# Optimization experiments

Measured on AMD Instinct MI355X. Metric: run time of the kernel, lower is better.

Reference implementation:

```python
import jax, jax.numpy as jnp
import numpy as np

B, C, H, W = 2048, 4, 84, 84
FEAT = 7 * 7 * 64  # 3136, from 84->20->9->7 conv arithmetic
D = 512
E = 6            # num_experts
K = 2            # top_k
A = 12           # output_dim (actions)


def _conv(x, w, b, stride):
    y = jax.lax.conv_general_dilated(
        x, w, window_strides=(stride, stride), padding='VALID',
        dimension_numbers=('NCHW', 'OIHW', 'NCHW'))
    return y + b[None, :, None, None]


def setup_inputs() -> dict:
    key = jax.random.key(0)
    ks = jax.random.split(key, 16)
    s = lambda k, shape, fan: jax.random.normal(k, shape, jnp.float32) * (1.0 / np.sqrt(fan))
    return {
        'x': jax.random.normal(ks[0], (B, C, H, W), jnp.float32),
        'c1_w': s(ks[1], (32, C, 8, 8), C * 64), 'c1_b': jnp.zeros((32,), jnp.float32),
        'c2_w': s(ks[2], (64, 32, 4, 4), 32 * 16), 'c2_b': jnp.zeros((64,), jnp.float32),
        'c3_w': s(ks[3], (64, 64, 3, 3), 64 * 9), 'c3_b': jnp.zeros((64,), jnp.float32),
        'fc_w': s(ks[4], (FEAT, D), FEAT), 'fc_b': jnp.zeros((D,), jnp.float32),
        'gate_w': s(ks[5], (D, E), D), 'gate_b': jnp.zeros((E,), jnp.float32),
        'e_w1': s(ks[6], (E, D, D), D), 'e_b1': jnp.zeros((E, D), jnp.float32),
        'e_w2': s(ks[7], (E, D, D), D), 'e_b2': jnp.zeros((E, D), jnp.float32),
        'e_w3': s(ks[8], (E, D, A), D), 'e_b3': jnp.zeros((E, A), jnp.float32),
    }


def reference(x, c1_w, c1_b, c2_w, c2_b, c3_w, c3_b, fc_w, fc_b,
              gate_w, gate_b, e_w1, e_b1, e_w2, e_b2, e_w3, e_b3):
    # CNN feature extractor (dropout omitted: eval semantics)
    h = jax.nn.relu(_conv(x, c1_w, c1_b, 4))
    h = jax.nn.relu(_conv(h, c2_w, c2_b, 2))
    h = jax.nn.relu(_conv(h, c3_w, c3_b, 1))
    h = h.reshape(h.shape[0], -1)                     # [B, 3136] (C,H,W flatten order)
    f = jax.nn.relu(h @ fc_w + fc_b)                  # [B, 512]

    # Gating: softmax -> top-2 -> renormalize
    gate_probs = jax.nn.softmax(f @ gate_w + gate_b, axis=-1)    # [B, E]
    top_p, top_i = jax.lax.top_k(gate_probs, K)                   # [B, K]
    top_p = top_p / jnp.sum(top_p, axis=-1, keepdims=True)

    # Experts: compute all (tiny MLPs), then gather top-k outputs
    h1 = jax.nn.relu(jnp.einsum('bd,edh->beh', f, e_w1) + e_b1)   # [B, E, D]
    h2 = jax.nn.relu(jnp.einsum('beh,ehg->beg', h1, e_w2) + e_b2) # [B, E, D]
    eo = jnp.einsum('beg,ego->beo', h2, e_w3) + e_b3              # [B, E, A]
    sel = jnp.take_along_axis(eo, top_i[:, :, None], axis=1)      # [B, K, A]
    out = jnp.sum(sel * top_p[:, :, None], axis=1)                # [B, A]
    return out
```

## Files before the change

### kernel.cpp

```cpp
#include <hip/hip_runtime.h>
#include <hip/hip_bf16.h>
#include <math.h>

typedef __attribute__((ext_vector_type(8))) short bf16x8;
typedef __attribute__((ext_vector_type(4))) float f32x4;

__device__ __forceinline__ float b2f(unsigned short u) {
    unsigned int v = ((unsigned int)u) << 16;
    return __uint_as_float(v);
}
__device__ __forceinline__ unsigned short f2b(float f) {
    __hip_bfloat16 h = __float2bfloat16(f);
    return *reinterpret_cast<unsigned short*>(&h);
}
__device__ __forceinline__ void split_trunc(float v, short& h, short& l) {
    unsigned int ui = __float_as_uint(v);
    h = (short)(ui >> 16);
    float hf = __uint_as_float(ui & 0xffff0000u);
    l = (short)f2b(v - hf);
}

__global__ __launch_bounds__(256) void prep_w(
    const float* __restrict__ w1, const float* __restrict__ w2, const float* __restrict__ w3,
    const float* __restrict__ ew3,
    unsigned short* __restrict__ wb1h, unsigned short* __restrict__ wb1l,
    unsigned short* __restrict__ w2h, unsigned short* __restrict__ w2l,
    unsigned short* __restrict__ w3h, unsigned short* __restrict__ w3l,
    float* __restrict__ w3t) {
    int tid = blockIdx.x * 256 + threadIdx.x;
    if (tid < 8192) {
        int k = tid >> 8, r = tid & 255;
        int c = r >> 6, ky = (r >> 3) & 7, kx = r & 7;
        float v = w1[tid];
        unsigned short h = f2b(v);
        int d = ((ky * 2 + (k >> 4)) * 16 + (k & 15)) * 32 + c * 8 + kx;
        wb1h[d] = h;
        wb1l[d] = f2b(v - b2f(h));
    } else if (tid < 8192 + 32768) {
        int i = tid - 8192;
        int n = i >> 9, r = i & 511;
        int c = r >> 4, ky = (r >> 2) & 3, kx = r & 3;
        float v = w2[i];
        unsigned short h = f2b(v);
        int d = ((ky * 4 + kx) * 64 + n) * 32 + c;
        w2h[d] = h;
        w2l[d] = f2b(v - b2f(h));
    } else if (tid < 8192 + 32768 + 36864) {
        int i = tid - 40960;
        int n = i / 576, r = i - n * 576;
        int c = r / 9, s = r - c * 9;
        int ky = s / 3, kx = s - ky * 3;
        float v = w3[i];
        unsigned short h = f2b(v);
        int d = (((ky * 3 + kx) * 2 + (c >> 5)) * 64 + n) * 32 + (c & 31);
        w3h[d] = h;
        w3l[d] = f2b(v - b2f(h));
    } else if (tid < 77824 + 36864) {
        int i = tid - 77824;
        int e = i / 6144, rem = i - e * 6144;
        int a = rem >> 9, k = rem & 511;
        w3t[i] = ew3[e * 6144 + k * 12 + a];
    }
}

__global__ __launch_bounds__(256) void prep_fcw(
    const float* __restrict__ fw, unsigned short* __restrict__ h, unsigned short* __restrict__ l) {
    __shared__ float tile[64][65];
    int k0 = blockIdx.x * 64;
    int n0 = blockIdx.y * 64;
    int tx = threadIdx.x & 63, ty = threadIdx.x >> 6;
#pragma unroll
    for (int j = 0; j < 16; j++) {
        int kk = ty + j * 4;
        int kp = k0 + kk;
        int p = kp >> 6, c = kp & 63;
        tile[kk][tx] = fw[(c * 49 + p) * 512 + n0 + tx];
    }
    __syncthreads();
#pragma unroll
    for (int j = 0; j < 16; j++) {
        int r = ty + j * 4;
        float v = tile[tx][r];
        unsigned short hh = f2b(v);
        long d = (long)(n0 + r) * 3136 + k0 + tx;
        h[d] = hh;
        l[d] = f2b(v - b2f(hh));
    }
}

__global__ __launch_bounds__(256) void prep_ewT(
    const float* __restrict__ ew1, const float* __restrict__ ew2,
    unsigned short* __restrict__ t1, unsigned short* __restrict__ t2) {
    __shared__ float tile[32][33];
    int z = blockIdx.z;
    int e = z % 6;
    const float* src = (z < 6) ? (ew1 + e * 262144) : (ew2 + e * 262144);
    unsigned short* dst = (z < 6) ? (t1 + e * 262144) : (t2 + e * 262144);
    int d0 = blockIdx.y * 32;
    int h0 = blockIdx.x * 32;
    int tx = threadIdx.x, ty = threadIdx.y;
#pragma unroll
    for (int j = 0; j < 4; j++)
        tile[ty + j * 8][tx] = src[(d0 + ty + j * 8) * 512 + h0 + tx];
    __syncthreads();
#pragma unroll
    for (int j = 0; j < 4; j++)
        dst[(h0 + ty + j * 8) * 512 + (d0 + tx)] = f2b(tile[tx][ty + j * 8]);
}

__global__ __launch_bounds__(256, 3) void conv1_k(
    const float* __restrict__ x, const unsigned short* __restrict__ wbh,
    const unsigned short* __restrict__ wbl, const float* __restrict__ b1,
    unsigned short* __restrict__ yhi, unsigned short* __restrict__ ylo) {
    int t = threadIdx.x;
    int wave = t >> 6, lane = t & 63, l16 = lane & 15, quad = lane >> 4;
    int px0 = blockIdx.x * 256 + wave * 64;
    const float* abase[4];
#pragma unroll
    for (int i = 0; i < 4; i++) {
        int px = px0 + i * 16 + l16;
        int n = px / 400;
        int rem = px - n * 400;
        int oy = rem / 20;
        int ox = rem - oy * 20;
        abase[i] = x + (long)n * 28224 + quad * 7056 + oy * 4 * 84 + ox * 4;
    }
    f32x4 acc[4][2];
#pragma unroll
    for (int i = 0; i < 4; i++)
#pragma unroll
        for (int j = 0; j < 2; j++)
#pragma unroll
            for (int r = 0; r < 4; r++) acc[i][j][r] = 0.f;
    float4 cur[8];
#pragma unroll
    for (int i = 0; i < 4; i++) {
        cur[i * 2] = *(const float4*)abase[i];
        cur[i * 2 + 1] = *(const float4*)(abase[i] + 4);
    }
#pragma unroll
    for (int ky = 0; ky < 8; ky++) {
        float4 nxt[8];
        if (ky < 7) {
#pragma unroll
            for (int i = 0; i < 4; i++) {
                const float* p = abase[i] + (ky + 1) * 84;
                nxt[i * 2] = *(const float4*)p;
                nxt[i * 2 + 1] = *(const float4*)(p + 4);
            }
        }
        int wo = (ky * 32 + l16) * 32 + quad * 8;
        bf16x8 bh0 = *(const bf16x8*)(wbh + wo);
        bf16x8 bh1 = *(const bf16x8*)(wbh + wo + 512);
        bf16x8 bl0 = *(const bf16x8*)(wbl + wo);
        bf16x8 bl1 = *(const bf16x8*)(wbl + wo + 512);
        bf16x8 ah[4], al[4];
#pragma unroll
        for (int i = 0; i < 4; i++) {
            float v[8] = {cur[i * 2].x, cur[i * 2].y, cur[i * 2].z, cur[i * 2].w,
                          cur[i * 2 + 1].x, cur[i * 2 + 1].y, cur[i * 2 + 1].z, cur[i * 2 + 1].w};
#pragma unroll
            for (int j = 0; j < 8; j++) {
                short hh, ll;
                split_trunc(v[j], hh, ll);
                ah[i][j] = hh;
                al[i][j] = ll;
            }
        }
#pragma unroll
        for (int i = 0; i < 4; i++) {
            acc[i][0] = __builtin_amdgcn_mfma_f32_16x16x32_bf16(ah[i], bh0, acc[i][0], 0, 0, 0);
            acc[i][0] = __builtin_amdgcn_mfma_f32_16x16x32_bf16(al[i], bh0, acc[i][0], 0, 0, 0);
            acc[i][0] = __builtin_amdgcn_mfma_f32_16x16x32_bf16(ah[i], bl0, acc[i][0], 0, 0, 0);
            acc[i][1] = __builtin_amdgcn_mfma_f32_16x16x32_bf16(ah[i], bh1, acc[i][1], 0, 0, 0);
            acc[i][1] = __builtin_amdgcn_mfma_f32_16x16x32_bf16(al[i], bh1, acc[i][1], 0, 0, 0);
            acc[i][1] = __builtin_amdgcn_mfma_f32_16x16x32_bf16(ah[i], bl1, acc[i][1], 0, 0, 0);
        }
        if (ky < 7) {
#pragma unroll
            for (int q = 0; q < 8; q++) cur[q] = nxt[q];
        }
    }
    float bias0 = b1[l16], bias1 = b1[16 + l16];
#pragma unroll
    for (int i = 0; i < 4; i++) {
#pragma unroll
        for (int r = 0; r < 4; r++) {
            long px = px0 + i * 16 + quad * 4 + r;
            long o = px * 32;
            float v0 = fmaxf(acc[i][0][r] + bias0, 0.f);
            float v1 = fmaxf(acc[i][1][r] + bias1, 0.f);
            short h0, l0, h1, l1;
            split_trunc(v0, h0, l0);
            split_trunc(v1, h1, l1);
            yhi[o + l16] = (unsigned short)h0;
            ylo[o + l16] = (unsigned short)l0;
            yhi[o + 16 + l16] = (unsigned short)h1;
            ylo[o + 16 + l16] = (unsigned short)l1;
        }
    }
}

template <int C, int IH, int IW, int OH, int OW, int S, int KH, int KW>
__global__ __launch_bounds__(64, 3) void convm_k(
    const unsigned short* __restrict__ xhi, const unsigned short* __restrict__ xlo,
    const unsigned short* __restrict__ whi, const unsigned short* __restrict__ wlo,
    const float* __restrict__ bias,
    unsigned short* __restrict__ yhi, unsigned short* __restrict__ ylo) {
    constexpr int CH = C / 32;
    constexpr int NCHUNK = KH * KW * CH;
    int lane = threadIdx.x, l16 = lane & 15, quad = lane >> 4;
    int pxbase = blockIdx.x * 64;
    long xoff[4];
#pragma unroll
    for (int i = 0; i < 4; i++) {
        int px = pxbase + i * 16 + l16;
        int n = px / (OH * OW);
        int rem = px - n * (OH * OW);
        int oy = rem / OW;
        int ox = rem - oy * OW;
        xoff[i] = (((long)n * IH + oy * S) * IW + ox * S) * C + quad * 8;
    }
    f32x4 acc[4][4];
#pragma unroll
    for (int i = 0; i < 4; i++)
#pragma unroll
        for (int j = 0; j < 4; j++)
#pragma unroll
            for (int r = 0; r < 4; r++) acc[i][j][r] = 0.f;
#pragma unroll 2
    for (int ck = 0; ck < NCHUNK; ck++) {
        int kyx = ck / CH;
        int ch = ck - kyx * CH;
        int ky = kyx / KW, kx = kyx - ky * KW;
        long koff = ((long)(ky * IW + kx)) * C + ch * 32;
        bf16x8 ah[4], al[4], bh[4], bl[4];
#pragma unroll
        for (int i = 0; i < 4; i++) {
            ah[i] = *(const bf16x8*)(xhi + xoff[i] + koff);
            al[i] = *(const bf16x8*)(xlo + xoff[i] + koff);
        }
#pragma unroll
        for (int j = 0; j < 4; j++) {
            long b = ((long)ck * 64 + j * 16 + l16) * 32 + quad * 8;
            bh[j] = *(const bf16x8*)(whi + b);
            bl[j] = *(const bf16x8*)(wlo + b);
        }
#pragma unroll
        for (int i = 0; i < 4; i++)
#pragma unroll
            for (int j = 0; j < 4; j++) {
                acc[i][j] = __builtin_amdgcn_mfma_f32_16x16x32_bf16(ah[i], bh[j], acc[i][j], 0, 0, 0);
                acc[i][j] = __builtin_amdgcn_mfma_f32_16x16x32_bf16(ah[i], bl[j], acc[i][j], 0, 0, 0);
                acc[i][j] = __builtin_amdgcn_mfma_f32_16x16x32_bf16(al[i], bh[j], acc[i][j], 0, 0, 0);
            }
    }
#pragma unroll
    for (int i = 0; i < 4; i++)
#pragma unroll
        for (int j = 0; j < 4; j++) {
            int col = j * 16 + l16;
            float bv = bias[col];
#pragma unroll
            for (int r = 0; r < 4; r++) {
                int prow = pxbase + i * 16 + quad * 4 + r;
                float v = fmaxf(acc[i][j][r] + bv, 0.f);
                unsigned short h = f2b(v);
                yhi[(long)prow * 64 + col] = h;
                ylo[(long)prow * 64 + col] = f2b(v - b2f(h));
            }
        }
}

__global__ __launch_bounds__(64, 3) void fc_k(
    const unsigned short* __restrict__ Ahi, const unsigned short* __restrict__ Alo,
    const unsigned short* __restrict__ Bhi, const unsigned short* __restrict__ Blo,
    float* __restrict__ Cp) {
    int lane = threadIdx.x, l16 = lane & 15, quad = lane >> 4;
    int m0 = blockIdx.x * 64, n0 = blockIdx.y * 64;
    int z = blockIdx.z;
    int kBase = z * 448;
    f32x4 acc[4][4];
#pragma unroll
    for (int i = 0; i < 4; i++)
#pragma unroll
        for (int j = 0; j < 4; j++)
#pragma unroll
            for (int r = 0; r < 4; r++) acc[i][j][r] = 0.f;
#pragma unroll 2
    for (int k0 = kBase; k0 < kBase + 448; k0 += 32) {
        bf16x8 ah[4], al[4], bh[4], bl[4];
#pragma unroll
        for (int i = 0; i < 4; i++) {
            long a = (long)(m0 + i * 16 + l16) * 3136 + k0 + quad * 8;
            ah[i] = *(const bf16x8*)(Ahi + a);
            al[i] = *(const bf16x8*)(Alo + a);
        }
#pragma unroll
        for (int j = 0; j < 4; j++) {
            long b = (long)(n0 + j * 16 + l16) * 3136 + k0 + quad * 8;
            bh[j] = *(const bf16x8*)(Bhi + b);
            bl[j] = *(const bf16x8*)(Blo + b);
        }
#pragma unroll
        for (int i = 0; i < 4; i++)
#pragma unroll
            for (int j = 0; j < 4; j++) {
                acc[i][j] = __builtin_amdgcn_mfma_f32_16x16x32_bf16(ah[i], bh[j], acc[i][j], 0, 0, 0);
                acc[i][j] = __builtin_amdgcn_mfma_f32_16x16x32_bf16(ah[i], bl[j], acc[i][j], 0, 0, 0);
                acc[i][j] = __builtin_amdgcn_mfma_f32_16x16x32_bf16(al[i], bh[j], acc[i][j], 0, 0, 0);
            }
    }
    float* Cz = Cp + (long)z * 1048576;
#pragma unroll
    for (int i = 0; i < 4; i++)
#pragma unroll
        for (int j = 0; j < 4; j++) {
            int col = n0 + j * 16 + l16;
#pragma unroll
            for (int r = 0; r < 4; r++) {
                int row = m0 + i * 16 + quad * 4 + r;
                Cz[row * 512 + col] = acc[i][j][r];
            }
        }
}

__global__ __launch_bounds__(256) void fc_fin(
    const float* __restrict__ Cp, const float* __restrict__ bias,
    float* __restrict__ f, unsigned short* __restrict__ fb) {
    int tid = blockIdx.x * 256 + threadIdx.x;
    int col = tid & 511;
    float v = bias[col];
#pragma unroll
    for (int z = 0; z < 7; z++) v += Cp[tid + (long)z * 1048576];
    v = fmaxf(v, 0.f);
    f[tid] = v;
    fb[tid] = f2b(v);
}

__global__ __launch_bounds__(256) void gate_k(
    const float* __restrict__ f, const float* __restrict__ gw, const float* __restrict__ gb,
    int* __restrict__ topi, float* __restrict__ topp) {
    int wave = threadIdx.x >> 6, lane = threadIdx.x & 63;
    int row = blockIdx.x * 4 + wave;
    float fv[8];
#pragma unroll
    for (int j = 0; j < 8; j++) fv[j] = f[row * 512 + lane + 64 * j];
    float lg[6];
#pragma unroll
    for (int e = 0; e < 6; e++) {
        float a = 0.f;
#pragma unroll
        for (int j = 0; j < 8; j++) a += fv[j] * gw[(lane + 64 * j) * 6 + e];
#pragma unroll
        for (int off = 32; off > 0; off >>= 1) a += __shfl_xor(a, off, 64);
        lg[e] = a + gb[e];
    }
    if (lane == 0) {
        int i1 = 0;
        float v1 = lg[0];
#pragma unroll
        for (int e = 1; e < 6; e++)
            if (lg[e] > v1) { v1 = lg[e]; i1 = e; }
        int i2 = (i1 == 0) ? 1 : 0;
        float v2 = lg[i2];
#pragma unroll
        for (int e = 0; e < 6; e++)
            if (e != i1 && lg[e] > v2) { v2 = lg[e]; i2 = e; }
        float pa = 1.f / (1.f + expf(v2 - v1));
        topi[row * 2] = i1;
        topi[row * 2 + 1] = i2;
        topp[row * 2] = pa;
        topp[row * 2 + 1] = 1.f - pa;
    }
}

__global__ __launch_bounds__(64, 4) void moe_gemm(
    const unsigned short* __restrict__ A, long aStride,
    const unsigned short* __restrict__ Bt, const float* __restrict__ bias,
    unsigned short* __restrict__ C) {
    int e = blockIdx.z;
    const unsigned short* Ae = A + (long)e * aStride;
    const unsigned short* Be = Bt + (long)e * 262144;
    const float* be = bias + e * 512;
    unsigned short* Ce = C + (long)e * 2048 * 512;
    int lane = threadIdx.x, l16 = lane & 15, quad = lane >> 4;
    int m0 = blockIdx.x * 64, n0 = blockIdx.y * 64;
    f32x4 acc[4][4];
#pragma unroll
    for (int i = 0; i < 4; i++)
#pragma unroll
        for (int j = 0; j < 4; j++)
#pragma unroll
            for (int r = 0; r < 4; r++) acc[i][j][r] = 0.f;
#pragma unroll 4
    for (int k0 = 0; k0 < 512; k0 += 32) {
        bf16x8 a[4], b[4];
#pragma unroll
        for (int i = 0; i < 4; i++)
            a[i] = *(const bf16x8*)(Ae + (long)(m0 + i * 16 + l16) * 512 + k0 + quad * 8);
#pragma unroll
        for (int j = 0; j < 4; j++)
            b[j] = *(const bf16x8*)(Be + (long)(n0 + j * 16 + l16) * 512 + k0 + quad * 8);
#pragma unroll
        for (int i = 0; i < 4; i++)
#pragma unroll
            for (int j = 0; j < 4; j++)
                acc[i][j] = __builtin_amdgcn_mfma_f32_16x16x32_bf16(a[i], b[j], acc[i][j], 0, 0, 0);
    }
#pragma unroll
    for (int i = 0; i < 4; i++)
#pragma unroll
        for (int j = 0; j < 4; j++) {
            int col = n0 + j * 16 + l16;
            float bcol = be[col];
#pragma unroll
            for (int r = 0; r < 4; r++) {
                int row = m0 + i * 16 + quad * 4 + r;
                float v = fmaxf(acc[i][j][r] + bcol, 0.f);
                Ce[(long)row * 512 + col] = f2b(v);
            }
        }
}

__global__ __launch_bounds__(256) void combine_k(
    const unsigned short* __restrict__ h2, const float* __restrict__ w3t,
    const float* __restrict__ b3, const int* __restrict__ topi,
    const float* __restrict__ topp, float* __restrict__ out) {
    int b = blockIdx.x * 4 + (threadIdx.x >> 6);
    int lane = threadIdx.x & 63;
    int e0 = topi[b * 2], e1 = topi[b * 2 + 1];
    float p0 = topp[b * 2], p1 = topp[b * 2 + 1];
    float r[12];
#pragma unroll
    for (int a = 0; a < 12; a++) r[a] = 0.f;
#pragma unroll
    for (int j = 0; j < 2; j++) {
        int e = j ? e1 : e0;
        float p = j ? p1 : p0;
        const unsigned short* hp = h2 + ((long)e * 2048 + b) * 512 + lane * 8;
        bf16x8 hv = *(const bf16x8*)hp;
        float hf[8];
#pragma unroll
        for (int q = 0; q < 8; q++) hf[q] = b2f((unsigned short)hv[q]);
        const float* wb = w3t + e * 6144 + lane * 8;
#pragma unroll
        for (int a = 0; a < 12; a++) {
            float4 w0 = *(const float4*)(wb + a * 512);
            float4 w1 = *(const float4*)(wb + a * 512 + 4);
            float acc = hf[0] * w0.x + hf[1] * w0.y + hf[2] * w0.z + hf[3] * w0.w +
                        hf[4] * w1.x + hf[5] * w1.y + hf[6] * w1.z + hf[7] * w1.w;
            r[a] += p * acc;
        }
    }
#pragma unroll
    for (int a = 0; a < 12; a++)
#pragma unroll
        for (int off = 32; off > 0; off >>= 1) r[a] += __shfl_xor(r[a], off, 64);
    float v = 0.f;
#pragma unroll
    for (int a = 0; a < 12; a++)
        if (lane == a) v = r[a];
    if (lane < 12)
        out[b * 12 + lane] = v + p0 * b3[e0 * 12 + lane] + p1 * b3[e1 * 12 + lane];
}

extern "C" void kernel_launch(void* const* d_in, const int* in_sizes, int n_in,
                              void* d_out, int out_size, void* d_ws, size_t ws_size,
                              hipStream_t stream) {
    const float* x   = (const float*)d_in[0];
    const float* c1w = (const float*)d_in[1];
    const float* c1b = (const float*)d_in[2];
    const float* c2w = (const float*)d_in[3];
    const float* c2b = (const float*)d_in[4];
    const float* c3w = (const float*)d_in[5];
    const float* c3b = (const float*)d_in[6];
    const float* fcw = (const float*)d_in[7];
    const float* fcb = (const float*)d_in[8];
    const float* gw  = (const float*)d_in[9];
    const float* gb  = (const float*)d_in[10];
    const float* ew1 = (const float*)d_in[11];
    const float* eb1 = (const float*)d_in[12];
    const float* ew2 = (const float*)d_in[13];
    const float* eb2 = (const float*)d_in[14];
    const float* ew3 = (const float*)d_in[15];
    const float* eb3 = (const float*)d_in[16];

    char* ws = (char*)d_ws;
    unsigned short* y1hi = (unsigned short*)(ws + 0L);
    unsigned short* y1lo = (unsigned short*)(ws + 52428800L);
    unsigned short* f3hi = (unsigned short*)(ws + 0L);
    unsigned short* f3lo = (unsigned short*)(ws + 12845056L);
    unsigned short* y2hi = (unsigned short*)(ws + 104857600L);
    unsigned short* y2lo = (unsigned short*)(ws + 126091264L);
    unsigned short* h1   = (unsigned short*)(ws + 104857600L);
    unsigned short* h2   = (unsigned short*)(ws + 117440512L);
    float* f             = (float*)(ws + 147324928L);
    unsigned short* fb   = (unsigned short*)(ws + 151519232L);
    int*   topi          = (int*)(ws + 153616384L);
    float* topp          = (float*)(ws + 153632768L);
    unsigned short* w2h  = (unsigned short*)(ws + 153681920L);
    unsigned short* w2l  = (unsigned short*)(ws + 153747456L);
    unsigned short* w3h  = (unsigned short*)(ws + 153812992L);
    unsigned short* w3l  = (unsigned short*)(ws + 153886720L);
    unsigned short* fcwh = (unsigned short*)(ws + 153960448L);
    unsigned short* fcwl = (unsigned short*)(ws + 157171712L);
    unsigned short* ew1t = (unsigned short*)(ws + 160382976L);
    unsigned short* ew2t = (unsigned short*)(ws + 163528704L);
    float* w3t           = (float*)(ws + 166674432L);
    float* Cp            = (float*)(ws + 166821888L);
    unsigned short* wb1h = (unsigned short*)(ws + 196182016L);
    unsigned short* wb1l = (unsigned short*)(ws + 196198400L);
    float* out = (float*)d_out;

    hipLaunchKernelGGL(prep_w, dim3(448), dim3(256), 0, stream, c1w, c2w, c3w, ew3,
                       wb1h, wb1l, w2h, w2l, w3h, w3l, w3t);
    hipLaunchKernelGGL(prep_fcw, dim3(49, 8), dim3(256), 0, stream, fcw, fcwh, fcwl);
    hipLaunchKernelGGL(prep_ewT, dim3(16, 16, 12), dim3(32, 8), 0, stream, ew1, ew2, ew1t, ew2t);
    hipLaunchKernelGGL(conv1_k, dim3(3200), dim3(256), 0, stream, x, wb1h, wb1l, c1b, y1hi, y1lo);
    hipLaunchKernelGGL((convm_k<32, 20, 20, 9, 9, 2, 4, 4>), dim3(2592), dim3(64), 0, stream,
                       y1hi, y1lo, w2h, w2l, c2b, y2hi, y2lo);
    hipLaunchKernelGGL((convm_k<64, 9, 9, 7, 7, 1, 3, 3>), dim3(1568), dim3(64), 0, stream,
                       y2hi, y2lo, w3h, w3l, c3b, f3hi, f3lo);
    hipLaunchKernelGGL(fc_k, dim3(32, 8, 7), dim3(64), 0, stream, f3hi, f3lo, fcwh, fcwl, Cp);
    hipLaunchKernelGGL(fc_fin, dim3(4096), dim3(256), 0, stream, Cp, fcb, f, fb);
    hipLaunchKernelGGL(gate_k, dim3(512), dim3(256), 0, stream, f, gw, gb, topi, topp);
    hipLaunchKernelGGL(moe_gemm, dim3(32, 8, 6), dim3(64), 0, stream, fb, 0L, ew1t, eb1, h1);
    hipLaunchKernelGGL(moe_gemm, dim3(32, 8, 6), dim3(64), 0, stream, h1, 1048576L, ew2t, eb2, h2);
    hipLaunchKernelGGL(combine_k, dim3(512), dim3(256), 0, stream, h2, w3t, eb3, topi, topp, out);
}
```

Baseline: 712.8 us.

## Route MoE GEMMs over only top-k selected rows and stage conv1 weights in LDS

The gate kernel now builds per-expert row lists with atomic counters and records each row's slot. The expert GEMMs then gather only the rows routed to each expert and exit early for empty tiles, so roughly a third of the dense all-expert work remains. Combine reads outputs by slot. Separately, conv1 preloads its bf16 hi/lo weight fragments into shared memory once per block instead of loading them from global memory on every ky iteration. In exchange the change adds atomics, a gather indirection, and reset of the counters in fc_fin.

```diff
diff --git a/kernel.cpp b/kernel.cpp
--- a/kernel.cpp
+++ b/kernel.cpp
@@ -112,7 +112,16 @@
     const float* __restrict__ x, const unsigned short* __restrict__ wbh,
     const unsigned short* __restrict__ wbl, const float* __restrict__ b1,
     unsigned short* __restrict__ yhi, unsigned short* __restrict__ ylo) {
+    __shared__ bf16x8 wlds[8][4][64];
     int t = threadIdx.x;
+    {
+        int tab = t >> 6, ln = t & 63;
+        const unsigned short* sb = ((tab < 2) ? wbh : wbl) +
+            ((ln & 15) * 32 + (ln >> 4) * 8 + (tab & 1) * 512);
+#pragma unroll
+        for (int k = 0; k < 8; k++)
+            wlds[k][tab][ln] = *(const bf16x8*)(sb + k * 1024);
+    }
     int wave = t >> 6, lane = t & 63, l16 = lane & 15, quad = lane >> 4;
     int px0 = blockIdx.x * 256 + wave * 64;
     const float* abase[4];
@@ -132,6 +141,7 @@
         for (int j = 0; j < 2; j++)
 #pragma unroll
             for (int r = 0; r < 4; r++) acc[i][j][r] = 0.f;
+    __syncthreads();
     float4 cur[8];
 #pragma unroll
     for (int i = 0; i < 4; i++) {
@@ -149,11 +159,10 @@
                 nxt[i * 2 + 1] = *(const float4*)(p + 4);
             }
         }
-        int wo = (ky * 32 + l16) * 32 + quad * 8;
-        bf16x8 bh0 = *(const bf16x8*)(wbh + wo);
-        bf16x8 bh1 = *(const bf16x8*)(wbh + wo + 512);
-        bf16x8 bl0 = *(const bf16x8*)(wbl + wo);
-        bf16x8 bl1 = *(const bf16x8*)(wbl + wo + 512);
+        bf16x8 bh0 = wlds[ky][0][lane];
+        bf16x8 bh1 = wlds[ky][1][lane];
+        bf16x8 bl0 = wlds[ky][2][lane];
+        bf16x8 bl1 = wlds[ky][3][lane];
         bf16x8 ah[4], al[4];
 #pragma unroll
         for (int i = 0; i < 4; i++) {
@@ -327,7 +336,8 @@
 
 __global__ __launch_bounds__(256) void fc_fin(
     const float* __restrict__ Cp, const float* __restrict__ bias,
-    float* __restrict__ f, unsigned short* __restrict__ fb) {
+    float* __restrict__ f, unsigned short* __restrict__ fb, int* __restrict__ cnt) {
+    if (blockIdx.x == 0 && threadIdx.x < 8) cnt[threadIdx.x] = 0;
     int tid = blockIdx.x * 256 + threadIdx.x;
     int col = tid & 511;
     float v = bias[col];
@@ -340,7 +350,8 @@
 
 __global__ __launch_bounds__(256) void gate_k(
     const float* __restrict__ f, const float* __restrict__ gw, const float* __restrict__ gb,
-    int* __restrict__ topi, float* __restrict__ topp) {
+    int* __restrict__ topi, float* __restrict__ topp,
+    int* __restrict__ cnt, int* __restrict__ rowlist, int* __restrict__ slotp) {
     int wave = threadIdx.x >> 6, lane = threadIdx.x & 63;
     int row = blockIdx.x * 4 + wave;
     float fv[8];
@@ -372,20 +383,36 @@
         topi[row * 2 + 1] = i2;
         topp[row * 2] = pa;
         topp[row * 2 + 1] = 1.f - pa;
+        int s1 = atomicAdd(cnt + i1, 1);
+        int s2 = atomicAdd(cnt + i2, 1);
+        rowlist[i1 * 2048 + s1] = row;
+        rowlist[i2 * 2048 + s2] = row;
+        slotp[row * 2] = s1;
+        slotp[row * 2 + 1] = s2;
     }
 }
 
 __global__ __launch_bounds__(64, 4) void moe_gemm(
     const unsigned short* __restrict__ A, long aStride,
     const unsigned short* __restrict__ Bt, const float* __restrict__ bias,
-    unsigned short* __restrict__ C) {
+    unsigned short* __restrict__ C,
+    const int* __restrict__ cnt, const int* __restrict__ rowlist) {
     int e = blockIdx.z;
+    int ne = cnt[e];
+    int m0 = blockIdx.x * 64;
+    if (m0 >= ne) return;
     const unsigned short* Ae = A + (long)e * aStride;
     const unsigned short* Be = Bt + (long)e * 262144;
     const float* be = bias + e * 512;
     unsigned short* Ce = C + (long)e * 2048 * 512;
     int lane = threadIdx.x, l16 = lane & 15, quad = lane >> 4;
-    int m0 = blockIdx.x * 64, n0 = blockIdx.y * 64;
+    int n0 = blockIdx.y * 64;
+    int arow[4];
+#pragma unroll
+    for (int i = 0; i < 4; i++) {
+        int slot = m0 + i * 16 + l16;
+        arow[i] = rowlist ? ((slot < ne) ? rowlist[e * 2048 + slot] : 0) : slot;
+    }
     f32x4 acc[4][4];
 #pragma unroll
     for (int i = 0; i < 4; i++)
@@ -398,7 +425,7 @@
         bf16x8 a[4], b[4];
 #pragma unroll
         for (int i = 0; i < 4; i++)
-            a[i] = *(const bf16x8*)(Ae + (long)(m0 + i * 16 + l16) * 512 + k0 + quad * 8);
+            a[i] = *(const bf16x8*)(Ae + (long)arow[i] * 512 + k0 + quad * 8);
 #pragma unroll
         for (int j = 0; j < 4; j++)
             b[j] = *(const bf16x8*)(Be + (long)(n0 + j * 16 + l16) * 512 + k0 + quad * 8);
@@ -426,19 +453,22 @@
 __global__ __launch_bounds__(256) void combine_k(
     const unsigned short* __restrict__ h2, const float* __restrict__ w3t,
     const float* __restrict__ b3, const int* __restrict__ topi,
-    const float* __restrict__ topp, float* __restrict__ out) {
+    const float* __restrict__ topp, const int* __restrict__ slotp,
+    float* __restrict__ out) {
     int b = blockIdx.x * 4 + (threadIdx.x >> 6);
     int lane = threadIdx.x & 63;
     int e0 = topi[b * 2], e1 = topi[b * 2 + 1];
     float p0 = topp[b * 2], p1 = topp[b * 2 + 1];
+    int s0 = slotp[b * 2], s1 = slotp[b * 2 + 1];
     float r[12];
 #pragma unroll
     for (int a = 0; a < 12; a++) r[a] = 0.f;
 #pragma unroll
     for (int j = 0; j < 2; j++) {
         int e = j ? e1 : e0;
+        int s = j ? s1 : s0;
         float p = j ? p1 : p0;
-        const unsigned short* hp = h2 + ((long)e * 2048 + b) * 512 + lane * 8;
+        const unsigned short* hp = h2 + ((long)e * 2048 + s) * 512 + lane * 8;
         bf16x8 hv = *(const bf16x8*)hp;
         float hf[8];
 #pragma unroll
@@ -491,6 +521,9 @@
     unsigned short* y1lo = (unsigned short*)(ws + 52428800L);
     unsigned short* f3hi = (unsigned short*)(ws + 0L);
     unsigned short* f3lo = (unsigned short*)(ws + 12845056L);
+    int*   cnt           = (int*)(ws + 26214400L);
+    int*   rowlist       = (int*)(ws + 26214464L);
+    int*   slotp         = (int*)(ws + 26263616L);
     unsigned short* y2hi = (unsigned short*)(ws + 104857600L);
     unsigned short* y2lo = (unsigned short*)(ws + 126091264L);
     unsigned short* h1   = (unsigned short*)(ws + 104857600L);
@@ -523,9 +556,13 @@
     hipLaunchKernelGGL((convm_k<64, 9, 9, 7, 7, 1, 3, 3>), dim3(1568), dim3(64), 0, stream,
                        y2hi, y2lo, w3h, w3l, c3b, f3hi, f3lo);
     hipLaunchKernelGGL(fc_k, dim3(32, 8, 7), dim3(64), 0, stream, f3hi, f3lo, fcwh, fcwl, Cp);
-    hipLaunchKernelGGL(fc_fin, dim3(4096), dim3(256), 0, stream, Cp, fcb, f, fb);
-    hipLaunchKernelGGL(gate_k, dim3(512), dim3(256), 0, stream, f, gw, gb, topi, topp);
-    hipLaunchKernelGGL(moe_gemm, dim3(32, 8, 6), dim3(64), 0, stream, fb, 0L, ew1t, eb1, h1);
-    hipLaunchKernelGGL(moe_gemm, dim3(32, 8, 6), dim3(64), 0, stream, h1, 1048576L, ew2t, eb2, h2);
-    hipLaunchKernelGGL(combine_k, dim3(512), dim3(256), 0, stream, h2, w3t, eb3, topi, topp, out);
-}
+    hipLaunchKernelGGL(fc_fin, dim3(4096), dim3(256), 0, stream, Cp, fcb, f, fb, cnt);
+    hipLaunchKernelGGL(gate_k, dim3(512), dim3(256), 0, stream, f, gw, gb, topi, topp,
+                       cnt, rowlist, slotp);
+    hipLaunchKernelGGL(moe_gemm, dim3(32, 8, 6), dim3(64), 0, stream, fb, 0L, ew1t, eb1, h1,
+                       cnt, rowlist);
+    hipLaunchKernelGGL(moe_gemm, dim3(32, 8, 6), dim3(64), 0, stream, h1, 1048576L, ew2t, eb2, h2,
+                       cnt, (const int*)nullptr);
+    hipLaunchKernelGGL(combine_k, dim3(512), dim3(256), 0, stream, h2, w3t, eb3, topi, topp,
+                       slotp, out);
+}
```

Result: slower. 734.8 us (+3.1%).
